# Kernel optimization log

Hardware: AMD Instinct MI355X
Metric: run time of the kernel (lower is better)

Reference implementation:

```python
import jax, jax.numpy as jnp
import numpy as np

B, T = 16, 64
A = 6              # num_actions
E = 12288          # embed_size
DET = 4096         # deter_size
HID = 1024         # hidden_size
S, D = 32, 32      # stoch_size, discrete
UM = 0.01          # uniform_mix
CLIP = 1.0         # action_clip
EPS = 1e-3         # LayerNorm eps


def _ln(x, g, b):
    m = jnp.mean(x, -1, keepdims=True)
    v = jnp.var(x, -1, keepdims=True)
    return (x - m) * jax.lax.rsqrt(v + EPS) * g + b


def setup_inputs() -> dict:
    key = jax.random.key(0)
    ks = jax.random.split(key, 24)
    w = lambda k, i, o: (jax.random.normal(k, (i, o), jnp.float32) / np.sqrt(i))
    gum = lambda k, shp: -jnp.log(-jnp.log(jax.random.uniform(k, shp, jnp.float32, 1e-6, 1.0 - 1e-6)))
    is_firsts = (jax.random.uniform(ks[2], (B, T)) < 0.05).astype(jnp.float32)
    is_firsts = is_firsts.at[:, 0].set(1.0)
    return {
        'embed': jax.random.normal(ks[0], (B, T, E), jnp.float32),
        'prev_actions': jax.random.normal(ks[1], (B, T, A), jnp.float32),
        'is_firsts': is_firsts,
        'gumbel_prior': gum(ks[3], (B, T, S, D)),
        'gumbel_post': gum(ks[4], (B, T, S, D)),
        'w_init': jnp.zeros((DET,), jnp.float32),
        'W_img1': w(ks[5], S * D + A, HID), 'g_img1': jnp.ones((HID,)), 'b_img1': jnp.zeros((HID,)),
        'W_gru': w(ks[6], HID + DET, 3 * DET), 'g_gru': jnp.ones((3 * DET,)), 'b_gru': jnp.zeros((3 * DET,)),
        'W_img2a': w(ks[7], DET, HID), 'g_img2': jnp.ones((HID,)), 'b_img2': jnp.zeros((HID,)),
        'W_img2b': w(ks[8], HID, S * D), 'bb_img2': jnp.zeros((S * D,)),
        'W_obs': w(ks[9], E + DET, HID), 'g_obs': jnp.ones((HID,)), 'b_obs': jnp.zeros((HID,)),
        'W_obsb': w(ks[10], HID, S * D), 'bb_obs': jnp.zeros((S * D,)),
    }


def reference(embed, prev_actions, is_firsts, gumbel_prior, gumbel_post,
              w_init, W_img1, g_img1, b_img1, W_gru, g_gru, b_gru,
              W_img2a, g_img2, b_img2, W_img2b, bb_img2,
              W_obs, g_obs, b_obs, W_obsb, bb_obs):
    sg = jax.lax.stop_gradient

    def clip_act(a):
        return a * sg(CLIP / jnp.maximum(jnp.abs(a), CLIP))

    def prior_logits(deter):  # mlp_img2
        h = jax.nn.silu(_ln(deter @ W_img2a, g_img2, b_img2))
        return (h @ W_img2b + bb_img2).reshape(deter.shape[:-1] + (S, D))

    def mix_probs(logits):  # OneHotDist uniform mix
        p = jax.nn.softmax(logits, -1)
        return (1.0 - UM) * p + UM / D

    def st_sample(logits, g):  # straight-through gumbel-max sample
        p = mix_probs(logits)
        oh = jax.nn.one_hot(jnp.argmax(jnp.log(p) + g, -1), D, dtype=logits.dtype)
        return oh + p - sg(p)

    def st_mode(logits):
        p = mix_probs(logits)
        oh = jax.nn.one_hot(jnp.argmax(p, -1), D, dtype=logits.dtype)
        return oh + p - sg(p)

    # learned initial state (initial(): deter=tanh(w), stoch=mode, logits=0)
    init_deter = jnp.broadcast_to(jnp.tanh(w_init)[None], (B, DET))
    init_stoch = st_mode(prior_logits(init_deter))

    # observe() with prev_state=None zeroes the first action and starts from initial state
    prev_actions = prev_actions.at[:, 0].set(0.0)

    def step(carry, xs):
        stoch, deter, logits_post = carry
        a, e, f, gp, gq = xs
        a = clip_act(a)                                  # clip in forward()
        f1 = f[:, None]
        f3 = f[:, None, None]
        a = a * (1.0 - f1)
        stoch = stoch * (1.0 - f3) + init_stoch * f3
        deter = deter * (1.0 - f1) + init_deter * f1
        logits_post = logits_post * (1.0 - f3)           # initial logits are zeros
        a = clip_act(a)                                  # clipped again in forward_img()
        # mlp_img1
        x = jax.nn.silu(_ln(jnp.concatenate([stoch.reshape(B, S * D), a], -1) @ W_img1, g_img1, b_img1))
        # DreamerV2 GRU cell: single LN-linear -> reset/cand/update
        parts = _ln(jnp.concatenate([x, deter], -1) @ W_gru, g_gru, b_gru)
        reset, cand, update = jnp.split(parts, 3, -1)
        reset = jax.nn.sigmoid(reset)
        cand = jnp.tanh(reset * cand)
        update = jax.nn.sigmoid(update - 1.0)
        deter_new = update * cand + (1.0 - update) * deter
        # prior head
        lp = prior_logits(deter_new)
        stoch_prior = st_sample(lp, gp)
        # posterior head (mlp_obs1)
        h2 = jax.nn.silu(_ln(jnp.concatenate([e, deter_new], -1) @ W_obs, g_obs, b_obs))
        lq = (h2 @ W_obsb + bb_obs).reshape(B, S, D)
        stoch_post = st_sample(lq, gq)
        return (stoch_post, deter_new, lq), (stoch_post, deter_new, lq, stoch_prior, lp)

    carry0 = (init_stoch, init_deter, jnp.zeros((B, S, D), embed.dtype))
    xs = (jnp.swapaxes(prev_actions, 0, 1), jnp.swapaxes(embed, 0, 1), jnp.swapaxes(is_firsts, 0, 1),
          jnp.swapaxes(gumbel_prior, 0, 1), jnp.swapaxes(gumbel_post, 0, 1))
    _, outs = jax.lax.scan(step, carry0, xs)
    post_stoch, post_deter, post_logits, prior_stoch, prior_lg = [jnp.swapaxes(o, 0, 1) for o in outs]
    # pack posts and priors (prior deter == post deter) into one array [B,T,8192]
    return jnp.concatenate([post_stoch.reshape(B, T, S * D), post_deter,
                            post_logits.reshape(B, T, S * D),
                            prior_stoch.reshape(B, T, S * D),
                            prior_lg.reshape(B, T, S * D)], -1)
```

## Files before the change

### kernel.cpp

```cpp
#include <hip/hip_runtime.h>
#include <cmath>


#define B 16
#define T_STEPS 64
#define A_DIM 6
#define E_DIM 12288
#define DET 4096
#define HID 1024
#define SD 1024
#define OUT_C 8192
#define OUT_RSTRIDE (T_STEPS * OUT_C)

typedef float f2v __attribute__((ext_vector_type(2)));
typedef float f4v __attribute__((ext_vector_type(4)));

__device__ __forceinline__ float block_sum(float v, float* red, int nw) {
#pragma unroll
  for (int m = 32; m >= 1; m >>= 1) v += __shfl_xor(v, m, 64);
  int wid = threadIdx.x >> 6;
  if ((threadIdx.x & 63) == 0) red[wid] = v;
  __syncthreads();
  if (wid == 0) {
    float s = ((int)threadIdx.x < nw) ? red[threadIdx.x] : 0.0f;
#pragma unroll
    for (int m = 8; m >= 1; m >>= 1) s += __shfl_xor(s, m, 16);
    if (threadIdx.x == 0) red[0] = s;
  }
  __syncthreads();
  float out = red[0];
  __syncthreads();
  return out;
}

__global__ __launch_bounds__(1024) void k_tanh(const float* __restrict__ w, float* __restrict__ o) {
  int i = blockIdx.x * 1024 + threadIdx.x;
  if (i < DET) o[i] = tanhf(w[i]);
}

__global__ __launch_bounds__(256) void k_prep(
    const float* __restrict__ isf, const float* __restrict__ pa, int t,
    const float* __restrict__ stoch_prev,
    const float* __restrict__ deter_prev, long deter_prev_stride,
    const float* __restrict__ init_stoch, const float* __restrict__ init_deter_row,
    float* __restrict__ stoch_in, float* __restrict__ deter_in, float* __restrict__ a_eff) {
  int r = blockIdx.x;
  float f = isf[r * T_STEPS + t];
  float omf = 1.0f - f;
  for (int c = threadIdx.x; c < SD; c += 256)
    stoch_in[r * SD + c] = stoch_prev[r * SD + c] * omf + init_stoch[r * SD + c] * f;
  for (int c = threadIdx.x; c < DET; c += 256)
    deter_in[r * DET + c] = deter_prev[(long)r * deter_prev_stride + c] * omf + init_deter_row[c] * f;
  if ((int)threadIdx.x < A_DIM) {
    float a = pa[(r * T_STEPS + t) * A_DIM + threadIdx.x];
    a = a * (1.0f / fmaxf(fabsf(a), 1.0f));
    a_eff[r * 8 + threadIdx.x] = a * omf;
  }
}

struct GemmArgs {
  const float* A0; long sA0; int cA0;
  const float* A1; long sA1;
  const float* W; int N; int Ktot; int KS; int nsplit;
  float* P;
};

template <bool NT>
__global__ __launch_bounds__(256) void k_gemm(GemmArgs g) {
  if ((int)blockIdx.y >= g.nsplit) return;
  const int tid = threadIdx.x;
  const int c0 = blockIdx.x * 512 + tid * 2;
  const int k0 = (int)blockIdx.y * g.KS;
  __shared__ float in_s[16][64];
  float acc[16][2];
#pragma unroll
  for (int r = 0; r < 16; r++) { acc[r][0] = 0.f; acc[r][1] = 0.f; }
  for (int kb = 0; kb < g.KS; kb += 64) {
    const int kbase = k0 + kb;
#pragma unroll
    for (int j = 0; j < 4; j++) {
      int ii = tid + j * 256;
      int r = ii >> 6, kk = ii & 63;
      int k = kbase + kk;
      float v = 0.f;
      if (k < g.cA0) v = g.A0[(long)r * g.sA0 + k];
      else if (k < g.Ktot) v = g.A1[(long)r * g.sA1 + (k - g.cA0)];
      in_s[r][kk] = v;
    }
    __syncthreads();
    if (kbase + 64 <= g.Ktot) {
      const float* wp = g.W + (size_t)kbase * g.N + c0;
#pragma unroll 4
      for (int kk = 0; kk < 64; kk++) {
        f2v w = NT ? __builtin_nontemporal_load((const f2v*)wp) : *(const f2v*)wp;
        wp += g.N;
#pragma unroll
        for (int r = 0; r < 16; r++) {
          acc[r][0] += in_s[r][kk] * w[0]; acc[r][1] += in_s[r][kk] * w[1];
        }
      }
    } else {
#pragma unroll 4
      for (int kk = 0; kk < 64; kk++) {
        int krow = kbase + kk; if (krow >= g.Ktot) krow = g.Ktot - 1;
        const f2v w = *(const f2v*)(g.W + (size_t)krow * g.N + c0);
#pragma unroll
        for (int r = 0; r < 16; r++) {
          acc[r][0] += in_s[r][kk] * w[0]; acc[r][1] += in_s[r][kk] * w[1];
        }
      }
    }
    __syncthreads();
  }
#pragma unroll
  for (int r = 0; r < 16; r++)
    *(f2v*)(g.P + ((size_t)blockIdx.y * 16 + r) * g.N + c0) = f2v{acc[r][0], acc[r][1]};
}

__global__ __launch_bounds__(1024) void k_fin(
    const float* __restrict__ P, int nP,
    const float* __restrict__ add, long ads,
    const float* __restrict__ gv, const float* __restrict__ bv,
    float* __restrict__ o) {
  int r = blockIdx.x, c = threadIdx.x;
  __shared__ float red[18];
  float v = add ? add[(size_t)r * ads + c] : 0.0f;
  for (int ks = 0; ks < nP; ks++) v += P[((size_t)ks * 16 + r) * HID + c];
  float m = block_sum(v, red, 16) * (1.0f / (float)HID);
  float d = v - m;
  float var = block_sum(d * d, red, 16) * (1.0f / (float)HID);
  float rs = 1.0f / sqrtf(var + 1e-3f);
  float y = d * rs * gv[c] + bv[c];
  float s = 1.0f / (1.0f + expf(-y));
  o[r * HID + c] = y * s;
}

__global__ __launch_bounds__(1024) void k_samp_init(
    const float* __restrict__ P, int nP, const float* __restrict__ bb,
    float* __restrict__ st) {
  int r = blockIdx.x, c = threadIdx.x;
  float acc = bb[c];
  for (int ks = 0; ks < nP; ks++) acc += P[((size_t)ks * 16 + r) * SD + c];
  int d = c & 31;
  float mx = acc;
#pragma unroll
  for (int m = 16; m >= 1; m >>= 1) mx = fmaxf(mx, __shfl_xor(mx, m, 32));
  float e = expf(acc - mx);
  float se = e;
#pragma unroll
  for (int m = 16; m >= 1; m >>= 1) se += __shfl_xor(se, m, 32);
  float p = 0.99f * (e / se) + 3.125e-4f;
  float by = p; int bi = d;
#pragma unroll
  for (int m = 16; m >= 1; m >>= 1) {
    float oy = __shfl_xor(by, m, 32);
    int oi = __shfl_xor(bi, m, 32);
    if (oy > by || (oy == by && oi < bi)) { by = oy; bi = oi; }
  }
  float oh = (d == bi) ? 1.0f : 0.0f;
  st[r * SD + c] = (oh + p) - p;
}

__global__ __launch_bounds__(256) void k_mm(const float* __restrict__ A, long lda,
                                            const float* __restrict__ Bw, int K,
                                            float* __restrict__ out, long ldo,
                                            const float* __restrict__ bias) {
  __shared__ float As[32][68];
  __shared__ float Bs[32][68];
  const int tid = threadIdx.x;
  const int tx = tid & 15, ty = tid >> 4;
  const int row0 = blockIdx.y * 64, col0 = blockIdx.x * 64;
  const int ar = tid >> 2, ak = (tid & 3) * 8;
  const int bk = tid >> 4, bc = (tid & 15) * 4;
  float acc[4][4] = {};
  const float* ap = A + (size_t)(row0 + ar) * lda + ak;
  const float* bp = Bw + (size_t)bk * HID + col0 + bc;
  for (int k0 = 0; k0 < K; k0 += 32) {
    float4 a0 = *(const float4*)(ap + k0);
    float4 a1 = *(const float4*)(ap + k0 + 4);
    float4 b0 = *(const float4*)(bp + (size_t)k0 * HID);
    float4 b1 = *(const float4*)(bp + (size_t)(k0 + 16) * HID);
    __syncthreads();
    As[ak + 0][ar] = a0.x; As[ak + 1][ar] = a0.y; As[ak + 2][ar] = a0.z; As[ak + 3][ar] = a0.w;
    As[ak + 4][ar] = a1.x; As[ak + 5][ar] = a1.y; As[ak + 6][ar] = a1.z; As[ak + 7][ar] = a1.w;
    *(float4*)&Bs[bk][bc] = b0;
    *(float4*)&Bs[bk + 16][bc] = b1;
    __syncthreads();
#pragma unroll
    for (int kk = 0; kk < 32; kk++) {
      float4 av = *(const float4*)&As[kk][ty * 4];
      float4 bv = *(const float4*)&Bs[kk][tx * 4];
      acc[0][0] += av.x * bv.x; acc[0][1] += av.x * bv.y; acc[0][2] += av.x * bv.z; acc[0][3] += av.x * bv.w;
      acc[1][0] += av.y * bv.x; acc[1][1] += av.y * bv.y; acc[1][2] += av.y * bv.z; acc[1][3] += av.y * bv.w;
      acc[2][0] += av.z * bv.x; acc[2][1] += av.z * bv.y; acc[2][2] += av.z * bv.z; acc[2][3] += av.z * bv.w;
      acc[3][0] += av.w * bv.x; acc[3][1] += av.w * bv.y; acc[3][2] += av.w * bv.z; acc[3][3] += av.w * bv.w;
    }
  }
#pragma unroll
  for (int i = 0; i < 4; i++) {
    float4 o;
    int col = col0 + tx * 4;
    o.x = acc[i][0] + (bias ? bias[col + 0] : 0.f);
    o.y = acc[i][1] + (bias ? bias[col + 1] : 0.f);
    o.z = acc[i][2] + (bias ? bias[col + 2] : 0.f);
    o.w = acc[i][3] + (bias ? bias[col + 3] : 0.f);
    *(float4*)(out + (size_t)(row0 + ty * 4 + i) * ldo + col) = o;
  }
}

__global__ __launch_bounds__(256) void k_ln_rows(float* __restrict__ h,
                                                 const float* __restrict__ gv,
                                                 const float* __restrict__ bv) {
  int row = blockIdx.x, c0 = threadIdx.x * 4;
  __shared__ float red[18];
  float4 v = *(const float4*)(h + (size_t)row * HID + c0);
  float lsum = (v.x + v.y) + (v.z + v.w);
  float m = block_sum(lsum, red, 4) * (1.0f / (float)HID);
  float dx = v.x - m, dy = v.y - m, dz = v.z - m, dw = v.w - m;
  float lv = (dx * dx + dy * dy) + (dz * dz + dw * dw);
  float var = block_sum(lv, red, 4) * (1.0f / (float)HID);
  float rs = 1.0f / sqrtf(var + 1e-3f);
  float4 o;
  float y0 = dx * rs * gv[c0] + bv[c0];         o.x = y0 / (1.0f + expf(-y0));
  float y1 = dy * rs * gv[c0 + 1] + bv[c0 + 1]; o.y = y1 / (1.0f + expf(-y1));
  float y2 = dz * rs * gv[c0 + 2] + bv[c0 + 2]; o.z = y2 / (1.0f + expf(-y2));
  float y3 = dw * rs * gv[c0 + 3] + bv[c0 + 3]; o.w = y3 / (1.0f + expf(-y3));
  *(float4*)(h + (size_t)row * HID + c0) = o;
}

__global__ __launch_bounds__(1024) void k_samp_prior(float* __restrict__ out,
                                                     const float* __restrict__ gum) {
  int m = blockIdx.x, c = threadIdx.x;
  float lp = out[(size_t)m * OUT_C + 7168 + c];
  int d = c & 31;
  float mx = lp;
#pragma unroll
  for (int mm = 16; mm >= 1; mm >>= 1) mx = fmaxf(mx, __shfl_xor(mx, mm, 32));
  float e = expf(lp - mx);
  float se = e;
#pragma unroll
  for (int mm = 16; mm >= 1; mm >>= 1) se += __shfl_xor(se, mm, 32);
  float p = 0.99f * (e / se) + 3.125e-4f;
  float y = logf(p) + gum[(size_t)m * SD + c];
  float by = y; int bi = d;
#pragma unroll
  for (int mm = 16; mm >= 1; mm >>= 1) {
    float oy = __shfl_xor(by, mm, 32);
    int oi = __shfl_xor(bi, mm, 32);
    if (oy > by || (oy == by && oi < bi)) { by = oy; bi = oi; }
  }
  float oh = (d == bi) ? 1.0f : 0.0f;
  out[(size_t)m * OUT_C + 6144 + c] = (oh + p) - p;
}

__global__ __launch_bounds__(256) void k_red(const float* __restrict__ P, int nP,
                                             float* __restrict__ S,
                                             float* __restrict__ red_s, float* __restrict__ red_q) {
  int chunk = blockIdx.x, r = blockIdx.y;
  int c = chunk * 1024 + threadIdx.x * 4;
  float4 s = {0, 0, 0, 0};
  for (int ks = 0; ks < nP; ks++) {
    float4 v = *(const float4*)(P + ((size_t)ks * 16 + r) * (3 * DET) + c);
    s.x += v.x; s.y += v.y; s.z += v.z; s.w += v.w;
  }
  *(float4*)(S + (size_t)r * (3 * DET) + c) = s;
  float sx = (s.x + s.y) + (s.z + s.w);
  float sq = (s.x * s.x + s.y * s.y) + (s.z * s.z + s.w * s.w);
  __shared__ float rbuf[8];
#pragma unroll
  for (int m = 32; m >= 1; m >>= 1) { sx += __shfl_xor(sx, m, 64); sq += __shfl_xor(sq, m, 64); }
  int wid = threadIdx.x >> 6;
  if ((threadIdx.x & 63) == 0) { rbuf[wid] = sx; rbuf[4 + wid] = sq; }
  __syncthreads();
  if (threadIdx.x == 0) {
    red_s[r * 12 + chunk] = (rbuf[0] + rbuf[1]) + (rbuf[2] + rbuf[3]);
    red_q[r * 12 + chunk] = (rbuf[4] + rbuf[5]) + (rbuf[6] + rbuf[7]);
  }
}

__global__ __launch_bounds__(256) void k_obsg(
    const float* __restrict__ Sg, const float* __restrict__ red_s, const float* __restrict__ red_q,
    const float* __restrict__ gg, const float* __restrict__ bg,
    const float* __restrict__ din_cur, float* __restrict__ din_next,
    const float* __restrict__ init_deter, const float* __restrict__ isf, int t,
    const float* __restrict__ W,
    float* __restrict__ out, float* __restrict__ P) {
  const int tid = threadIdx.x;
  const int tile = blockIdx.x;
  const int split = blockIdx.y;
  const int c0 = tile * 512 + tid * 2;
  const int j0 = split * 128;
  __shared__ float dn_s[16][128];
  __shared__ float mvf[16][3];
  if (tid < 16) {
    int r = tid;
    float s = 0.f, q = 0.f;
    for (int k2 = 0; k2 < 12; k2++) { s += red_s[r * 12 + k2]; q += red_q[r * 12 + k2]; }
    float m = s * (1.0f / (float)(3 * DET));
    float var = q * (1.0f / (float)(3 * DET)) - m * m;
    mvf[r][0] = m; mvf[r][1] = 1.0f / sqrtf(var + 1e-3f);
    mvf[r][2] = (t + 1 < T_STEPS) ? isf[r * T_STEPS + t + 1] : 0.0f;
  }
  __syncthreads();
  for (int e = tid; e < 16 * 128; e += 256) {
    int r = e >> 7, jj = e & 127;
    int j = j0 + jj;
    float m = mvf[r][0], rs = mvf[r][1];
    const float* Sr = Sg + (size_t)r * (3 * DET);
    float lr = (Sr[j] - m) * rs * gg[j] + bg[j];
    float lc = (Sr[j + DET] - m) * rs * gg[j + DET] + bg[j + DET];
    float lu = (Sr[j + 2 * DET] - m) * rs * gg[j + 2 * DET] + bg[j + 2 * DET];
    float rr = 1.0f / (1.0f + expf(-lr));
    float cd = tanhf(rr * lc);
    float uu = 1.0f / (1.0f + expf(-(lu - 1.0f)));
    float dn = uu * cd + (1.0f - uu) * din_cur[r * DET + j];
    dn_s[r][jj] = dn;
    if (tile == 0) {
      out[(size_t)(r * T_STEPS + t) * OUT_C + 1024 + j] = dn;
      float ft = mvf[r][2];
      din_next[r * DET + j] = dn * (1.0f - ft) + init_deter[j] * ft;
    }
  }
  __syncthreads();
  float acc[16][2];
#pragma unroll
  for (int r = 0; r < 16; r++) { acc[r][0] = 0.f; acc[r][1] = 0.f; }
  for (int kb = 0; kb < 128; kb += 64) {
    const float* wp = W + (size_t)(j0 + kb) * HID + c0;
#pragma unroll 4
    for (int kk = 0; kk < 64; kk++) {
      f2v w = __builtin_nontemporal_load((const f2v*)wp);
      wp += HID;
#pragma unroll
      for (int r = 0; r < 16; r++) {
        float iv = dn_s[r][kb + kk];
        acc[r][0] += iv * w[0]; acc[r][1] += iv * w[1];
      }
    }
  }
#pragma unroll
  for (int r = 0; r < 16; r++)
    *(f2v*)(P + ((size_t)split * 16 + r) * HID + c0) = f2v{acc[r][0], acc[r][1]};
}

__global__ __launch_bounds__(1024) void k_samp(
    const float* __restrict__ P, int nP, const float* __restrict__ bb,
    const float* __restrict__ gum, long gs,
    float* __restrict__ st, long ss, float* __restrict__ lg, long ls,
    const float* __restrict__ isf, const float* __restrict__ pa, int t,
    float* __restrict__ stoch_in, float* __restrict__ a_eff,
    const float* __restrict__ init_stoch) {
  int r = blockIdx.x, c = threadIdx.x;
  float acc = bb[c];
  for (int ks = 0; ks < nP; ks++) acc += P[((size_t)ks * 16 + r) * SD + c];
  int d = c & 31;
  float mx = acc;
#pragma unroll
  for (int m = 16; m >= 1; m >>= 1) mx = fmaxf(mx, __shfl_xor(mx, m, 32));
  float e = expf(acc - mx);
  float se = e;
#pragma unroll
  for (int m = 16; m >= 1; m >>= 1) se += __shfl_xor(se, m, 32);
  float p = 0.99f * (e / se) + 3.125e-4f;
  float y = logf(p) + gum[(long)r * gs + c];
  float by = y; int bi = d;
#pragma unroll
  for (int m = 16; m >= 1; m >>= 1) {
    float oy = __shfl_xor(by, m, 32);
    int oi = __shfl_xor(bi, m, 32);
    if (oy > by || (oy == by && oi < bi)) { by = oy; bi = oi; }
  }
  float oh = (d == bi) ? 1.0f : 0.0f;
  float outv = (oh + p) - p;
  st[(long)r * ss + c] = outv;
  lg[(long)r * ls + c] = acc;
  float fn = (t + 1 < T_STEPS) ? isf[r * T_STEPS + t + 1] : 0.0f;
  stoch_in[r * SD + c] = outv * (1.0f - fn) + init_stoch[r * SD + c] * fn;
  if (c < A_DIM) {
    float a = (t + 1 < T_STEPS) ? pa[(r * T_STEPS + t + 1) * A_DIM + c] : 0.0f;
    a = a * (1.0f / fmaxf(fabsf(a), 1.0f));
    a_eff[r * 8 + c] = a * (1.0f - fn);
  }
}

static inline GemmArgs mkargs(const float* A0, long sA0, int cA0,
                              const float* A1, long sA1,
                              const float* W, int N, int Ktot, int KS, int nsplit, float* P) {
  GemmArgs g; g.A0 = A0; g.sA0 = sA0; g.cA0 = cA0; g.A1 = A1; g.sA1 = sA1;
  g.W = W; g.N = N; g.Ktot = Ktot; g.KS = KS; g.nsplit = nsplit; g.P = P;
  return g;
}

extern "C" void kernel_launch(void* const* d_in, const int* in_sizes, int n_in,
                              void* d_out, int out_size, void* d_ws, size_t ws_size,
                              hipStream_t stream) {
  const float* embed  = (const float*)d_in[0];
  const float* pa     = (const float*)d_in[1];
  const float* isf    = (const float*)d_in[2];
  const float* gprior = (const float*)d_in[3];
  const float* gpost  = (const float*)d_in[4];
  const float* w_init = (const float*)d_in[5];
  const float* W1  = (const float*)d_in[6];
  const float* g1  = (const float*)d_in[7];
  const float* b1  = (const float*)d_in[8];
  const float* Wg  = (const float*)d_in[9];
  const float* gg  = (const float*)d_in[10];
  const float* bg  = (const float*)d_in[11];
  const float* W2a = (const float*)d_in[12];
  const float* g2  = (const float*)d_in[13];
  const float* b2  = (const float*)d_in[14];
  const float* W2b = (const float*)d_in[15];
  const float* bb2 = (const float*)d_in[16];
  const float* Wo  = (const float*)d_in[17];
  const float* go  = (const float*)d_in[18];
  const float* bo  = (const float*)d_in[19];
  const float* Wob = (const float*)d_in[20];
  const float* bbo = (const float*)d_in[21];
  float* out = (float*)d_out;
  float* ws  = (float*)d_ws;

  const size_t STATE_FLOATS = 196608 + 512 + 200832;
  int NSPLIT = 40, KSG = 128;
  if (ws_size < ((size_t)40 * 16 * 12288 + STATE_FLOATS) * 4) { NSPLIT = 20; KSG = 256; }
  const size_t ASZ = (size_t)NSPLIT * 16 * 12288;

  float* arena = ws;
  float* Pg    = arena;
  float* h_all = arena;
  float* Pimg1 = arena;
  float* Pb    = arena + ASZ - 786432;
  float* Ps1   = arena + ASZ - 262144;
  float* Sg    = arena + ASZ;
  float* red_s = Sg + 196608;
  float* red_q = red_s + 192;
  float* st_   = red_s + 512;
  float* init_stoch = st_;
  float* init_deter = st_ + 16384;
  float* stoch_in   = st_ + 20480;
  float* din0       = st_ + 36864;
  float* din1       = st_ + 102400;
  float* a_eff      = st_ + 167936;
  float* x          = st_ + 168064;
  float* h2         = st_ + 184448;

  k_mm<<<dim3(16, 16), 256, 0, stream>>>(embed, E_DIM, Wo, E_DIM, out + 5120, OUT_C, nullptr);

  k_tanh<<<4, 1024, 0, stream>>>(w_init, init_deter);
  k_gemm<true><<<dim3(2, 32), 256, 0, stream>>>(
      mkargs(init_deter, 0, DET, nullptr, 0, W2a, HID, DET, 128, 32, Pb));
  k_fin<<<16, 1024, 0, stream>>>(Pb, 32, nullptr, 0, g2, b2, x);
  k_gemm<true><<<dim3(2, 16), 256, 0, stream>>>(
      mkargs(x, HID, HID, nullptr, 0, W2b, SD, HID, 64, 16, Ps1));
  k_samp_init<<<16, 1024, 0, stream>>>(Ps1, 16, bb2, init_stoch);

  k_prep<<<16, 256, 0, stream>>>(isf, pa, 0, init_stoch, init_deter, 0,
                                 init_stoch, init_deter, stoch_in, din0, a_eff);

  const float* Wo2 = Wo + (size_t)E_DIM * HID;
  for (int t = 0; t < T_STEPS; t++) {
    float* din_cur  = (t & 1) ? din1 : din0;
    float* din_next = (t & 1) ? din0 : din1;
    k_gemm<true><<<dim3(2, 17), 256, 0, stream>>>(
        mkargs(stoch_in, SD, SD, a_eff, 8, W1, HID, SD + A_DIM, 64, 17, Pimg1));
    k_fin<<<16, 1024, 0, stream>>>(Pimg1, 17, nullptr, 0, g1, b1, x);
    k_gemm<false><<<dim3(24, NSPLIT), 256, 0, stream>>>(
        mkargs(x, HID, HID, din_cur, DET, Wg, 3 * DET, HID + DET, KSG, NSPLIT, Pg));
    k_red<<<dim3(12, 16), 256, 0, stream>>>(Pg, NSPLIT, Sg, red_s, red_q);
    k_obsg<<<dim3(2, 32), 256, 0, stream>>>(Sg, red_s, red_q, gg, bg, din_cur, din_next,
                                            init_deter, isf, t, Wo2, out, Pb);
    k_fin<<<16, 1024, 0, stream>>>(Pb, 32, out + (size_t)t * OUT_C + 5120, OUT_RSTRIDE,
                                   go, bo, h2);
    k_gemm<true><<<dim3(2, 16), 256, 0, stream>>>(
        mkargs(h2, HID, HID, nullptr, 0, Wob, SD, HID, 64, 16, Ps1));
    k_samp<<<16, 1024, 0, stream>>>(
        Ps1, 16, bbo, gpost + (size_t)t * SD, (long)T_STEPS * SD,
        out + (size_t)t * OUT_C + 0, OUT_RSTRIDE,
        out + (size_t)t * OUT_C + 5120, OUT_RSTRIDE,
        isf, pa, t, stoch_in, a_eff, init_stoch);
  }

  k_mm<<<dim3(16, 16), 256, 0, stream>>>(out + 1024, OUT_C, W2a, DET, h_all, HID, nullptr);
  k_ln_rows<<<1024, 256, 0, stream>>>(h_all, g2, b2);
  k_mm<<<dim3(16, 16), 256, 0, stream>>>(h_all, HID, W2b, HID, out + 7168, OUT_C, bb2);
  k_samp_prior<<<1024, 1024, 0, stream>>>(out, gprior);
}
```

Before: 12.04 ms.

## Fold prior head into per-step loop alongside posterior head kernels

After: 10.49 ms. -12.9%, faster.

```diff
diff --git a/kernel.cpp b/kernel.cpp
--- a/kernel.cpp
+++ b/kernel.cpp
@@ -14,6 +14,8 @@
 
 typedef float f2v __attribute__((ext_vector_type(2)));
 typedef float f4v __attribute__((ext_vector_type(4)));
+
+#define NTL(p) __builtin_nontemporal_load(p)
 
 __device__ __forceinline__ float block_sum(float v, float* red, int nw) {
 #pragma unroll
@@ -66,7 +68,8 @@
 };
 
 template <bool NT>
-__global__ __launch_bounds__(256) void k_gemm(GemmArgs g) {
+__global__ __launch_bounds__(256) void k_gemm(GemmArgs ga, GemmArgs gb) {
+  const GemmArgs g = blockIdx.z ? gb : ga;
   if ((int)blockIdx.y >= g.nsplit) return;
   const int tid = threadIdx.x;
   const int c0 = blockIdx.x * 512 + tid * 2;
@@ -92,7 +95,7 @@
       const float* wp = g.W + (size_t)kbase * g.N + c0;
 #pragma unroll 4
       for (int kk = 0; kk < 64; kk++) {
-        f2v w = NT ? __builtin_nontemporal_load((const f2v*)wp) : *(const f2v*)wp;
+        f2v w = NT ? NTL((const f2v*)wp) : *(const f2v*)wp;
         wp += g.N;
 #pragma unroll
         for (int r = 0; r < 16; r++) {
@@ -117,12 +120,19 @@
     *(f2v*)(g.P + ((size_t)blockIdx.y * 16 + r) * g.N + c0) = f2v{acc[r][0], acc[r][1]};
 }
 
-__global__ __launch_bounds__(1024) void k_fin(
-    const float* __restrict__ P, int nP,
-    const float* __restrict__ add, long ads,
-    const float* __restrict__ gv, const float* __restrict__ bv,
-    float* __restrict__ o) {
-  int r = blockIdx.x, c = threadIdx.x;
+__global__ __launch_bounds__(1024) void k_fin2(
+    const float* __restrict__ Pa_, int nPa, const float* __restrict__ addA, long adsA,
+    const float* __restrict__ gva, const float* __restrict__ bva, float* __restrict__ oa,
+    const float* __restrict__ Pb_, int nPb, const float* __restrict__ addB, long adsB,
+    const float* __restrict__ gvb, const float* __restrict__ bvb, float* __restrict__ ob) {
+  int which = blockIdx.x >> 4, r = blockIdx.x & 15, c = threadIdx.x;
+  const float* P = which ? Pb_ : Pa_;
+  int nP = which ? nPb : nPa;
+  const float* add = which ? addB : addA;
+  long ads = which ? adsB : adsA;
+  const float* gv = which ? gvb : gva;
+  const float* bv = which ? bvb : bva;
+  float* o = which ? ob : oa;
   __shared__ float red[18];
   float v = add ? add[(size_t)r * ads + c] : 0.0f;
   for (int ks = 0; ks < nP; ks++) v += P[((size_t)ks * 16 + r) * HID + c];
@@ -163,8 +173,7 @@
 
 __global__ __launch_bounds__(256) void k_mm(const float* __restrict__ A, long lda,
                                             const float* __restrict__ Bw, int K,
-                                            float* __restrict__ out, long ldo,
-                                            const float* __restrict__ bias) {
+                                            float* __restrict__ out, long ldo) {
   __shared__ float As[32][68];
   __shared__ float Bs[32][68];
   const int tid = threadIdx.x;
@@ -198,59 +207,11 @@
   }
 #pragma unroll
   for (int i = 0; i < 4; i++) {
+    int col = col0 + tx * 4;
     float4 o;
-    int col = col0 + tx * 4;
-    o.x = acc[i][0] + (bias ? bias[col + 0] : 0.f);
-    o.y = acc[i][1] + (bias ? bias[col + 1] : 0.f);
-    o.z = acc[i][2] + (bias ? bias[col + 2] : 0.f);
-    o.w = acc[i][3] + (bias ? bias[col + 3] : 0.f);
+    o.x = acc[i][0]; o.y = acc[i][1]; o.z = acc[i][2]; o.w = acc[i][3];
     *(float4*)(out + (size_t)(row0 + ty * 4 + i) * ldo + col) = o;
   }
-}
-
-__global__ __launch_bounds__(256) void k_ln_rows(float* __restrict__ h,
-                                                 const float* __restrict__ gv,
-                                                 const float* __restrict__ bv) {
-  int row = blockIdx.x, c0 = threadIdx.x * 4;
-  __shared__ float red[18];
-  float4 v = *(const float4*)(h + (size_t)row * HID + c0);
-  float lsum = (v.x + v.y) + (v.z + v.w);
-  float m = block_sum(lsum, red, 4) * (1.0f / (float)HID);
-  float dx = v.x - m, dy = v.y - m, dz = v.z - m, dw = v.w - m;
-  float lv = (dx * dx + dy * dy) + (dz * dz + dw * dw);
-  float var = block_sum(lv, red, 4) * (1.0f / (float)HID);
-  float rs = 1.0f / sqrtf(var + 1e-3f);
-  float4 o;
-  float y0 = dx * rs * gv[c0] + bv[c0];         o.x = y0 / (1.0f + expf(-y0));
-  float y1 = dy * rs * gv[c0 + 1] + bv[c0 + 1]; o.y = y1 / (1.0f + expf(-y1));
-  float y2 = dz * rs * gv[c0 + 2] + bv[c0 + 2]; o.z = y2 / (1.0f + expf(-y2));
-  float y3 = dw * rs * gv[c0 + 3] + bv[c0 + 3]; o.w = y3 / (1.0f + expf(-y3));
-  *(float4*)(h + (size_t)row * HID + c0) = o;
-}
-
-__global__ __launch_bounds__(1024) void k_samp_prior(float* __restrict__ out,
-                                                     const float* __restrict__ gum) {
-  int m = blockIdx.x, c = threadIdx.x;
-  float lp = out[(size_t)m * OUT_C + 7168 + c];
-  int d = c & 31;
-  float mx = lp;
-#pragma unroll
-  for (int mm = 16; mm >= 1; mm >>= 1) mx = fmaxf(mx, __shfl_xor(mx, mm, 32));
-  float e = expf(lp - mx);
-  float se = e;
-#pragma unroll
-  for (int mm = 16; mm >= 1; mm >>= 1) se += __shfl_xor(se, mm, 32);
-  float p = 0.99f * (e / se) + 3.125e-4f;
-  float y = logf(p) + gum[(size_t)m * SD + c];
-  float by = y; int bi = d;
-#pragma unroll
-  for (int mm = 16; mm >= 1; mm >>= 1) {
-    float oy = __shfl_xor(by, mm, 32);
-    int oi = __shfl_xor(bi, mm, 32);
-    if (oy > by || (oy == by && oi < bi)) { by = oy; bi = oi; }
-  }
-  float oh = (d == bi) ? 1.0f : 0.0f;
-  out[(size_t)m * OUT_C + 6144 + c] = (oh + p) - p;
 }
 
 __global__ __launch_bounds__(256) void k_red(const float* __restrict__ P, int nP,
@@ -278,16 +239,20 @@
   }
 }
 
-__global__ __launch_bounds__(256) void k_obsg(
+__global__ __launch_bounds__(256) void k_obsg2(
     const float* __restrict__ Sg, const float* __restrict__ red_s, const float* __restrict__ red_q,
     const float* __restrict__ gg, const float* __restrict__ bg,
     const float* __restrict__ din_cur, float* __restrict__ din_next,
     const float* __restrict__ init_deter, const float* __restrict__ isf, int t,
-    const float* __restrict__ W,
-    float* __restrict__ out, float* __restrict__ P) {
+    const float* __restrict__ W0, float* __restrict__ P0,
+    const float* __restrict__ W1p, float* __restrict__ P1p,
+    float* __restrict__ out) {
   const int tid = threadIdx.x;
   const int tile = blockIdx.x;
   const int split = blockIdx.y;
+  const int z = blockIdx.z;
+  const float* W = z ? W1p : W0;
+  float* P = z ? P1p : P0;
   const int c0 = tile * 512 + tid * 2;
   const int j0 = split * 128;
   __shared__ float dn_s[16][128];
@@ -315,7 +280,7 @@
     float uu = 1.0f / (1.0f + expf(-(lu - 1.0f)));
     float dn = uu * cd + (1.0f - uu) * din_cur[r * DET + j];
     dn_s[r][jj] = dn;
-    if (tile == 0) {
+    if (z == 0 && tile == 0) {
       out[(size_t)(r * T_STEPS + t) * OUT_C + 1024 + j] = dn;
       float ft = mvf[r][2];
       din_next[r * DET + j] = dn * (1.0f - ft) + init_deter[j] * ft;
@@ -329,7 +294,7 @@
     const float* wp = W + (size_t)(j0 + kb) * HID + c0;
 #pragma unroll 4
     for (int kk = 0; kk < 64; kk++) {
-      f2v w = __builtin_nontemporal_load((const f2v*)wp);
+      f2v w = NTL((const f2v*)wp);
       wp += HID;
 #pragma unroll
       for (int r = 0; r < 16; r++) {
@@ -343,15 +308,21 @@
     *(f2v*)(P + ((size_t)split * 16 + r) * HID + c0) = f2v{acc[r][0], acc[r][1]};
 }
 
-__global__ __launch_bounds__(1024) void k_samp(
-    const float* __restrict__ P, int nP, const float* __restrict__ bb,
-    const float* __restrict__ gum, long gs,
-    float* __restrict__ st, long ss, float* __restrict__ lg, long ls,
-    const float* __restrict__ isf, const float* __restrict__ pa, int t,
+__global__ __launch_bounds__(1024) void k_samp2(
+    const float* __restrict__ P0, const float* __restrict__ bb0,
+    const float* __restrict__ gum0, long gs0,
+    const float* __restrict__ P1, const float* __restrict__ bb1,
+    const float* __restrict__ gum1, long gs1,
+    float* __restrict__ out, int t, int nP,
+    const float* __restrict__ isf, const float* __restrict__ pa,
     float* __restrict__ stoch_in, float* __restrict__ a_eff,
     const float* __restrict__ init_stoch) {
-  int r = blockIdx.x, c = threadIdx.x;
-  float acc = bb[c];
+  int which = blockIdx.x >> 4, r = blockIdx.x & 15, c = threadIdx.x;
+  const float* P = which ? P1 : P0;
+  const float* bbv = which ? bb1 : bb0;
+  const float* gum = which ? gum1 : gum0;
+  long gs = which ? gs1 : gs0;
+  float acc = bbv[c];
   for (int ks = 0; ks < nP; ks++) acc += P[((size_t)ks * 16 + r) * SD + c];
   int d = c & 31;
   float mx = acc;
@@ -372,14 +343,20 @@
   }
   float oh = (d == bi) ? 1.0f : 0.0f;
   float outv = (oh + p) - p;
-  st[(long)r * ss + c] = outv;
-  lg[(long)r * ls + c] = acc;
-  float fn = (t + 1 < T_STEPS) ? isf[r * T_STEPS + t + 1] : 0.0f;
-  stoch_in[r * SD + c] = outv * (1.0f - fn) + init_stoch[r * SD + c] * fn;
-  if (c < A_DIM) {
-    float a = (t + 1 < T_STEPS) ? pa[(r * T_STEPS + t + 1) * A_DIM + c] : 0.0f;
-    a = a * (1.0f / fmaxf(fabsf(a), 1.0f));
-    a_eff[r * 8 + c] = a * (1.0f - fn);
+  float* ob = out + (size_t)t * OUT_C + (size_t)r * OUT_RSTRIDE;
+  if (which) {
+    ob[c] = outv;
+    ob[5120 + c] = acc;
+    float fn = (t + 1 < T_STEPS) ? isf[r * T_STEPS + t + 1] : 0.0f;
+    stoch_in[r * SD + c] = outv * (1.0f - fn) + init_stoch[r * SD + c] * fn;
+    if (c < A_DIM) {
+      float a = (t + 1 < T_STEPS) ? pa[(r * T_STEPS + t + 1) * A_DIM + c] : 0.0f;
+      a = a * (1.0f / fmaxf(fabsf(a), 1.0f));
+      a_eff[r * 8 + c] = a * (1.0f - fn);
+    }
+  } else {
+    ob[6144 + c] = outv;
+    ob[7168 + c] = acc;
   }
 }
 
@@ -419,18 +396,13 @@
   float* out = (float*)d_out;
   float* ws  = (float*)d_ws;
 
-  const size_t STATE_FLOATS = 196608 + 512 + 200832;
-  int NSPLIT = 40, KSG = 128;
-  if (ws_size < ((size_t)40 * 16 * 12288 + STATE_FLOATS) * 4) { NSPLIT = 20; KSG = 256; }
-  const size_t ASZ = (size_t)NSPLIT * 16 * 12288;
-
-  float* arena = ws;
-  float* Pg    = arena;
-  float* h_all = arena;
-  float* Pimg1 = arena;
-  float* Pb    = arena + ASZ - 786432;
-  float* Ps1   = arena + ASZ - 262144;
-  float* Sg    = arena + ASZ;
+  float* Pg    = ws;
+  float* Pimg1 = ws;
+  float* Pa    = ws + 278528;
+  float* Pb    = ws + 802816;
+  float* Ps0   = ws + 1327104;
+  float* Ps1   = ws + 1589248;
+  float* Sg    = ws + 3932160;
   float* red_s = Sg + 196608;
   float* red_q = red_s + 192;
   float* st_   = red_s + 512;
@@ -441,16 +413,20 @@
   float* din1       = st_ + 102400;
   float* a_eff      = st_ + 167936;
   float* x          = st_ + 168064;
-  float* h2         = st_ + 184448;
-
-  k_mm<<<dim3(16, 16), 256, 0, stream>>>(embed, E_DIM, Wo, E_DIM, out + 5120, OUT_C, nullptr);
+  float* h          = st_ + 184448;
+  float* h2         = st_ + 200832;
+
+  GemmArgs Z = mkargs(nullptr, 0, 0, nullptr, 0, nullptr, 1, 0, 64, 0, nullptr);
+
+  k_mm<<<dim3(16, 16), 256, 0, stream>>>(embed, E_DIM, Wo, E_DIM, out + 5120, OUT_C);
 
   k_tanh<<<4, 1024, 0, stream>>>(w_init, init_deter);
-  k_gemm<true><<<dim3(2, 32), 256, 0, stream>>>(
-      mkargs(init_deter, 0, DET, nullptr, 0, W2a, HID, DET, 128, 32, Pb));
-  k_fin<<<16, 1024, 0, stream>>>(Pb, 32, nullptr, 0, g2, b2, x);
-  k_gemm<true><<<dim3(2, 16), 256, 0, stream>>>(
-      mkargs(x, HID, HID, nullptr, 0, W2b, SD, HID, 64, 16, Ps1));
+  k_gemm<true><<<dim3(2, 32, 1), 256, 0, stream>>>(
+      mkargs(init_deter, 0, DET, nullptr, 0, W2a, HID, DET, 128, 32, Pb), Z);
+  k_fin2<<<16, 1024, 0, stream>>>(Pb, 32, nullptr, 0, g2, b2, x,
+                                  Pb, 32, nullptr, 0, g2, b2, x);
+  k_gemm<true><<<dim3(2, 16, 1), 256, 0, stream>>>(
+      mkargs(x, HID, HID, nullptr, 0, W2b, SD, HID, 64, 16, Ps1), Z);
   k_samp_init<<<16, 1024, 0, stream>>>(Ps1, 16, bb2, init_stoch);
 
   k_prep<<<16, 256, 0, stream>>>(isf, pa, 0, init_stoch, init_deter, 0,
@@ -460,27 +436,24 @@
   for (int t = 0; t < T_STEPS; t++) {
     float* din_cur  = (t & 1) ? din1 : din0;
     float* din_next = (t & 1) ? din0 : din1;
-    k_gemm<true><<<dim3(2, 17), 256, 0, stream>>>(
-        mkargs(stoch_in, SD, SD, a_eff, 8, W1, HID, SD + A_DIM, 64, 17, Pimg1));
-    k_fin<<<16, 1024, 0, stream>>>(Pimg1, 17, nullptr, 0, g1, b1, x);
-    k_gemm<false><<<dim3(24, NSPLIT), 256, 0, stream>>>(
-        mkargs(x, HID, HID, din_cur, DET, Wg, 3 * DET, HID + DET, KSG, NSPLIT, Pg));
-    k_red<<<dim3(12, 16), 256, 0, stream>>>(Pg, NSPLIT, Sg, red_s, red_q);
-    k_obsg<<<dim3(2, 32), 256, 0, stream>>>(Sg, red_s, red_q, gg, bg, din_cur, din_next,
-                                            init_deter, isf, t, Wo2, out, Pb);
-    k_fin<<<16, 1024, 0, stream>>>(Pb, 32, out + (size_t)t * OUT_C + 5120, OUT_RSTRIDE,
-                                   go, bo, h2);
-    k_gemm<true><<<dim3(2, 16), 256, 0, stream>>>(
+    k_gemm<true><<<dim3(2, 17, 1), 256, 0, stream>>>(
+        mkargs(stoch_in, SD, SD, a_eff, 8, W1, HID, SD + A_DIM, 64, 17, Pimg1), Z);
+    k_fin2<<<16, 1024, 0, stream>>>(Pimg1, 17, nullptr, 0, g1, b1, x,
+                                    Pimg1, 17, nullptr, 0, g1, b1, x);
+    k_gemm<false><<<dim3(24, 20, 1), 256, 0, stream>>>(
+        mkargs(x, HID, HID, din_cur, DET, Wg, 3 * DET, HID + DET, 256, 20, Pg), Z);
+    k_red<<<dim3(12, 16), 256, 0, stream>>>(Pg, 20, Sg, red_s, red_q);
+    k_obsg2<<<dim3(2, 32, 2), 256, 0, stream>>>(Sg, red_s, red_q, gg, bg, din_cur, din_next,
+                                                init_deter, isf, t, Wo2, Pb, W2a, Pa, out);
+    k_fin2<<<32, 1024, 0, stream>>>(Pa, 32, nullptr, 0, g2, b2, h,
+                                    Pb, 32, out + (size_t)t * OUT_C + 5120, OUT_RSTRIDE,
+                                    go, bo, h2);
+    k_gemm<true><<<dim3(2, 16, 2), 256, 0, stream>>>(
+        mkargs(h, HID, HID, nullptr, 0, W2b, SD, HID, 64, 16, Ps0),
         mkargs(h2, HID, HID, nullptr, 0, Wob, SD, HID, 64, 16, Ps1));
-    k_samp<<<16, 1024, 0, stream>>>(
-        Ps1, 16, bbo, gpost + (size_t)t * SD, (long)T_STEPS * SD,
-        out + (size_t)t * OUT_C + 0, OUT_RSTRIDE,
-        out + (size_t)t * OUT_C + 5120, OUT_RSTRIDE,
-        isf, pa, t, stoch_in, a_eff, init_stoch);
-  }
-
-  k_mm<<<dim3(16, 16), 256, 0, stream>>>(out + 1024, OUT_C, W2a, DET, h_all, HID, nullptr);
-  k_ln_rows<<<1024, 256, 0, stream>>>(h_all, g2, b2);
-  k_mm<<<dim3(16, 16), 256, 0, stream>>>(h_all, HID, W2b, HID, out + 7168, OUT_C, bb2);
-  k_samp_prior<<<1024, 1024, 0, stream>>>(out, gprior);
-}
+    k_samp2<<<32, 1024, 0, stream>>>(
+        Ps0, bb2, gprior + (size_t)t * SD, (long)T_STEPS * SD,
+        Ps1, bbo, gpost + (size_t)t * SD, (long)T_STEPS * SD,
+        out, t, 16, isf, pa, stoch_in, a_eff, init_stoch);
+  }
+}
```
